# Kernel tuning notes

Hardware: AMD Instinct MI355X
Metric: run time of the kernel (lower is better)

The kernel has to match this reference:

```python
import jax, jax.numpy as jnp
import numpy as np

M_DIM = 1024
H_DIM = 1024
NEG = -1e9


def setup_inputs() -> dict:
    key = jax.random.key(0)
    ks = jax.random.split(key, 9)
    B, S = 4, 2048
    q = jax.random.normal(ks[0], (B, S, M_DIM), dtype=jnp.float32)
    k = jax.random.normal(ks[1], (B, S, M_DIM), dtype=jnp.float32)
    v = jax.random.normal(ks[2], (B, S, M_DIM), dtype=jnp.float32)
    attention_mask = jnp.ones((B, S), dtype=jnp.int32)
    sc = 1.0 / np.sqrt(M_DIM)
    Wq_w = jax.random.normal(ks[3], (H_DIM, M_DIM), dtype=jnp.float32) * sc
    Wq_b = jnp.zeros((H_DIM,), dtype=jnp.float32)
    Wk_w = jax.random.normal(ks[4], (H_DIM, M_DIM), dtype=jnp.float32) * sc
    Wk_b = jnp.zeros((H_DIM,), dtype=jnp.float32)
    Wv_w = jax.random.normal(ks[5], (H_DIM, M_DIM), dtype=jnp.float32) * sc
    Wv_b = jnp.zeros((H_DIM,), dtype=jnp.float32)
    return {"q": q, "k": k, "v": v, "attention_mask": attention_mask,
            "Wq_w": Wq_w, "Wq_b": Wq_b, "Wk_w": Wk_w, "Wk_b": Wk_b,
            "Wv_w": Wv_w, "Wv_b": Wv_b}


def reference(q, k, v, attention_mask, Wq_w, Wq_b, Wk_w, Wk_b, Wv_w, Wv_b):
    # Linear projections (torch Linear: x @ W.T + b)
    qh = jnp.einsum('bsm,hm->bsh', q, Wq_w) + Wq_b
    kh = jnp.einsum('bsm,hm->bsh', k, Wk_w) + Wk_b
    vh = jnp.einsum('bsm,hm->bsh', v, Wv_w) + Wv_b
    # Scaled dot-product scores: [B, Sq, Sk]
    scores = jnp.einsum('bqh,bkh->bqk', qh, kh) / jnp.sqrt(jnp.float32(H_DIM))
    # Padding mask: attention_mask [B, Sk] -> [B, 1, Sk]
    pad = attention_mask.astype(bool)[:, None, :]
    scores = jnp.where(pad, scores, NEG)
    # Causal mask (apply_mask=True)
    Sq, Sk = scores.shape[1], scores.shape[2]
    causal = jnp.tril(jnp.ones((Sq, Sk), dtype=bool))
    scores = jnp.where(causal[None, :, :], scores, NEG)
    attn = jax.nn.softmax(scores, axis=-1)
    out = jnp.einsum('bqk,bkh->bqh', attn, vh)
    # dropout is identity in eval mode
    return out
```

## Files before the change

### kernel.cpp

```cpp
#include <hip/hip_runtime.h>
#include <stdint.h>


typedef __attribute__((ext_vector_type(8))) short s8v;
typedef __attribute__((ext_vector_type(4))) float f4v;

__device__ __forceinline__ unsigned short f2bf(float f) {
    union { float f; unsigned u; } v; v.f = f;
    unsigned u = v.u;
    u = u + 0x7fffu + ((u >> 16) & 1u);
    return (unsigned short)(u >> 16);
}

__device__ __forceinline__ void gld_lds16(const void* gptr, void* lptr) {
    __builtin_amdgcn_global_load_lds(
        (const __attribute__((address_space(1))) unsigned int*)(uintptr_t)gptr,
        (__attribute__((address_space(3))) unsigned int*)(unsigned int)(uintptr_t)lptr,
        16, 0, 0);
}

__global__ __launch_bounds__(256) void convert_all(
    const float* __restrict__ q, const float* __restrict__ k, const float* __restrict__ v,
    const float* __restrict__ wq, const float* __restrict__ wk, const float* __restrict__ wv,
    unsigned short* __restrict__ qb, unsigned short* __restrict__ kb, unsigned short* __restrict__ vb,
    unsigned short* __restrict__ wqb, unsigned short* __restrict__ wkb, unsigned short* __restrict__ wvb,
    float* __restrict__ l)
{
    int b = blockIdx.x;
    if (b >= 27648) {
        int li = (b - 27648) * 256 + threadIdx.x;
        l[li] = 0.f;
        return;
    }
    const float* src; unsigned short* dst; int blk;
    if (b < 8192)       { src = q;  dst = qb;  blk = b; }
    else if (b < 16384) { src = k;  dst = kb;  blk = b - 8192; }
    else if (b < 24576) { src = v;  dst = vb;  blk = b - 16384; }
    else if (b < 25600) { src = wq; dst = wqb; blk = b - 24576; }
    else if (b < 26624) { src = wk; dst = wkb; blk = b - 25600; }
    else                { src = wv; dst = wvb; blk = b - 26624; }
    size_t idx = (size_t)blk * 1024 + (size_t)threadIdx.x * 4;
    float4 f = *(const float4*)(src + idx);
    ushort4 o = make_ushort4(f2bf(f.x), f2bf(f.y), f2bf(f.z), f2bf(f.w));
    *(ushort4*)(dst + idx) = o;
}

__device__ __forceinline__ void gemm_tiles(
    const unsigned short* __restrict__ A, int lda,
    const unsigned short* __restrict__ Bt, int ldb,
    int m0, int n0, int kTiles,
    unsigned short* As, unsigned short* Bs,
    f4v acc[4][4])
{
    const int t    = threadIdx.x;
    const int lane = t & 63;
    const int wave = t >> 6;
    const int wm   = (wave >> 1) * 64;
    const int wn   = (wave & 1) * 64;
    const int l15  = lane & 15;
    const int quad = lane >> 4;

    const int c0 = t, c1 = t + 256;
    unsigned short* As0 = As + (c0 & ~63) * 8;
    unsigned short* As1 = As + (c1 & ~63) * 8;
    unsigned short* Bs0 = Bs + (c0 & ~63) * 8;
    unsigned short* Bs1 = Bs + (c1 & ~63) * 8;
    const unsigned short* Ag0 = A  + (size_t)(m0 + (c0 >> 2)) * lda + (c0 & 3) * 8;
    const unsigned short* Ag1 = A  + (size_t)(m0 + (c1 >> 2)) * lda + (c1 & 3) * 8;
    const unsigned short* Bg0 = Bt + (size_t)(n0 + (c0 >> 2)) * ldb + (c0 & 3) * 8;
    const unsigned short* Bg1 = Bt + (size_t)(n0 + (c1 >> 2)) * ldb + (c1 & 3) * 8;

    const unsigned short* a_base = As + quad * 8;
    const unsigned short* b_base = Bs + quad * 8;

    gld_lds16(Ag0, As0);
    gld_lds16(Ag1, As1);
    gld_lds16(Bg0, Bs0);
    gld_lds16(Bg1, Bs1);

    for (int kt = 0; kt < kTiles; ++kt) {
        __syncthreads();
        Ag0 += 32; Ag1 += 32; Bg0 += 32; Bg1 += 32;
        if (kt + 1 < kTiles) {
            const int nb = ((kt + 1) & 1) * 4096;
            gld_lds16(Ag0, As0 + nb);
            gld_lds16(Ag1, As1 + nb);
            gld_lds16(Bg0, Bs0 + nb);
            gld_lds16(Bg1, Bs1 + nb);
        }
        const int cb = (kt & 1) * 4096;
        s8v af[4], bf[4];
        #pragma unroll
        for (int i = 0; i < 4; ++i)
            af[i] = *(const s8v*)(a_base + cb + (wm + i * 16 + l15) * 32);
        #pragma unroll
        for (int j = 0; j < 4; ++j)
            bf[j] = *(const s8v*)(b_base + cb + (wn + j * 16 + l15) * 32);
        #pragma unroll
        for (int i = 0; i < 4; ++i)
            #pragma unroll
            for (int j = 0; j < 4; ++j)
                acc[i][j] = __builtin_amdgcn_mfma_f32_16x16x32_bf16(af[i], bf[j], acc[i][j], 0, 0, 0);
    }
}

#define ACC_INIT  f4v acc[4][4]; { f4v z = {0.f,0.f,0.f,0.f}; \
    _Pragma("unroll") for (int i = 0; i < 4; ++i) \
    _Pragma("unroll") for (int j = 0; j < 4; ++j) acc[i][j] = z; }

#define LANE_VARS \
    const int lane = threadIdx.x & 63; const int wave = threadIdx.x >> 6; \
    const int wm = (wave >> 1) * 64;  const int wn = (wave & 1) * 64; \
    const int l15 = lane & 15;        const int quad = lane >> 4;

__global__ __launch_bounds__(512, 2) void proj_kernel(
    const unsigned short* __restrict__ qb, const unsigned short* __restrict__ wqb,
    const float* __restrict__ bq, unsigned short* __restrict__ QH,
    const unsigned short* __restrict__ kb, const unsigned short* __restrict__ wkb,
    const float* __restrict__ bk, unsigned short* __restrict__ KH,
    const unsigned short* __restrict__ vb, const unsigned short* __restrict__ wvb,
    const float* __restrict__ bv, unsigned short* __restrict__ VHT)
{
    const int z = blockIdx.z;
    const unsigned short* X; const unsigned short* W; const float* bias; unsigned short* Y;
    if (z == 0)      { X = qb; W = wqb; bias = bq; Y = QH; }
    else if (z == 1) { X = kb; W = wkb; bias = bk; Y = KH; }
    else             { X = vb; W = wvb; bias = bv; Y = VHT; }

    __shared__ __align__(16) unsigned short As[2 * 256 * 64];
    __shared__ __align__(16) unsigned short Bs[2 * 256 * 64];

    const int t    = threadIdx.x;
    const int lane = t & 63;
    const int w    = t >> 6;
    const int wm   = (w >> 2) * 128;
    const int wn   = (w & 3) * 64;
    const int l15  = lane & 15;
    const int quad = lane >> 4;
    const int m0   = blockIdx.x * 256;
    const int n0   = blockIdx.y * 256;
    enum { KT = 16 };

    const int r0 = t >> 3;
    const int sw = (t & 7) ^ (r0 & 7);
    const unsigned short* gA = X + (size_t)(m0 + r0) * 1024 + sw * 8;
    const unsigned short* gB = W + (size_t)(n0 + r0) * 1024 + sw * 8;
    unsigned short* lA = As + (t & ~63) * 8;
    unsigned short* lB = Bs + (t & ~63) * 8;

#define PSTAGE_A(b, h, kt) { \
    gld_lds16(gA + (size_t)(h) * 131072 + (kt) * 64,         lA + (b) * 16384 + (h) * 8192); \
    gld_lds16(gA + (size_t)(h) * 131072 + 65536 + (kt) * 64, lA + (b) * 16384 + (h) * 8192 + 4096); }
#define PSTAGE_B(b, h, kt) { \
    gld_lds16(gB + (size_t)(h) * 131072 + (kt) * 64,         lB + (b) * 16384 + (h) * 8192); \
    gld_lds16(gB + (size_t)(h) * 131072 + 65536 + (kt) * 64, lB + (b) * 16384 + (h) * 8192 + 4096); }

    const int aoff = (wm + l15) * 64;
    const int boff = (wn + l15) * 64;
    const int seg0 = ((quad    ) ^ (l15 & 7)) * 8;
    const int seg1 = ((quad | 4) ^ (l15 & 7)) * 8;

    f4v acc[8][4];
    { f4v zz = {0.f, 0.f, 0.f, 0.f};
      #pragma unroll
      for (int i = 0; i < 8; ++i)
        #pragma unroll
        for (int j = 0; j < 4; ++j) acc[i][j] = zz; }
    s8v a[8], b0[4], b1[4];

    PSTAGE_A(0, 0, 0); PSTAGE_A(0, 1, 0); PSTAGE_B(0, 0, 0); PSTAGE_B(0, 1, 0);
    PSTAGE_B(1, 0, 1); PSTAGE_A(1, 0, 1);
    asm volatile("s_waitcnt vmcnt(4)" ::: "memory");
    __builtin_amdgcn_s_barrier();

    for (int kt = 0; kt < KT; ++kt) {
        const int p  = kt & 1;
        const int np = p ^ 1;
        const unsigned short* Ar = As + p * 16384 + aoff;
        const unsigned short* Br = Bs + p * 16384 + boff;

        #pragma unroll
        for (int i = 0; i < 4; ++i) {
            a[i * 2]     = *(const s8v*)(Ar + i * 1024 + seg0);
            a[i * 2 + 1] = *(const s8v*)(Ar + i * 1024 + seg1);
        }
        #pragma unroll
        for (int j = 0; j < 2; ++j) {
            b0[j * 2]     = *(const s8v*)(Br + j * 1024 + seg0);
            b0[j * 2 + 1] = *(const s8v*)(Br + j * 1024 + seg1);
        }
        #pragma unroll
        for (int j = 0; j < 2; ++j) {
            b1[j * 2]     = *(const s8v*)(Br + 2048 + j * 1024 + seg0);
            b1[j * 2 + 1] = *(const s8v*)(Br + 2048 + j * 1024 + seg1);
        }
        if (kt + 1 < KT) PSTAGE_A(np, 1, kt + 1);
        __builtin_amdgcn_s_setprio(1);
        #pragma unroll
        for (int i = 0; i < 4; ++i)
            #pragma unroll
            for (int j = 0; j < 2; ++j) {
                acc[i][j] = __builtin_amdgcn_mfma_f32_16x16x32_bf16(a[i*2],   b0[j*2],   acc[i][j], 0, 0, 0);
                acc[i][j] = __builtin_amdgcn_mfma_f32_16x16x32_bf16(a[i*2+1], b0[j*2+1], acc[i][j], 0, 0, 0);
            }
        __builtin_amdgcn_s_setprio(0);
        if (kt + 1 < KT) PSTAGE_B(np, 1, kt + 1);
        __builtin_amdgcn_s_setprio(1);
        #pragma unroll
        for (int i = 0; i < 4; ++i)
            #pragma unroll
            for (int j = 0; j < 2; ++j) {
                acc[i][2+j] = __builtin_amdgcn_mfma_f32_16x16x32_bf16(a[i*2],   b1[j*2],   acc[i][2+j], 0, 0, 0);
                acc[i][2+j] = __builtin_amdgcn_mfma_f32_16x16x32_bf16(a[i*2+1], b1[j*2+1], acc[i][2+j], 0, 0, 0);
            }
        __builtin_amdgcn_s_setprio(0);
        #pragma unroll
        for (int i = 0; i < 4; ++i) {
            a[i * 2]     = *(const s8v*)(Ar + 4096 + i * 1024 + seg0);
            a[i * 2 + 1] = *(const s8v*)(Ar + 4096 + i * 1024 + seg1);
        }
        __builtin_amdgcn_s_barrier();
        if (kt + 2 < KT) PSTAGE_B(p, 0, kt + 2);
        __builtin_amdgcn_s_setprio(1);
        #pragma unroll
        for (int i = 0; i < 4; ++i)
            #pragma unroll
            for (int j = 0; j < 2; ++j) {
                acc[4+i][2+j] = __builtin_amdgcn_mfma_f32_16x16x32_bf16(a[i*2],   b1[j*2],   acc[4+i][2+j], 0, 0, 0);
                acc[4+i][2+j] = __builtin_amdgcn_mfma_f32_16x16x32_bf16(a[i*2+1], b1[j*2+1], acc[4+i][2+j], 0, 0, 0);
            }
        __builtin_amdgcn_s_setprio(0);
        __builtin_amdgcn_s_barrier();
        if (kt + 2 < KT) PSTAGE_A(p, 0, kt + 2);
        __builtin_amdgcn_s_setprio(1);
        #pragma unroll
        for (int i = 0; i < 4; ++i)
            #pragma unroll
            for (int j = 0; j < 2; ++j) {
                acc[4+i][j] = __builtin_amdgcn_mfma_f32_16x16x32_bf16(a[i*2],   b0[j*2],   acc[4+i][j], 0, 0, 0);
                acc[4+i][j] = __builtin_amdgcn_mfma_f32_16x16x32_bf16(a[i*2+1], b0[j*2+1], acc[4+i][j], 0, 0, 0);
            }
        __builtin_amdgcn_s_setprio(0);
        if (kt + 2 < KT) { asm volatile("s_waitcnt vmcnt(4)" ::: "memory"); }
        else             { asm volatile("s_waitcnt vmcnt(0)" ::: "memory"); }
        __builtin_amdgcn_s_barrier();
    }
#undef PSTAGE_A
#undef PSTAGE_B

    #pragma unroll
    for (int ig = 0; ig < 8; ++ig) {
        int row = m0 + wm + ig * 16 + quad * 4;
        #pragma unroll
        for (int jg = 0; jg < 4; ++jg) {
            int col = n0 + wn + jg * 16 + l15;
            float bvv = bias[col];
            if (z != 2) {
                #pragma unroll
                for (int r = 0; r < 4; ++r)
                    Y[(size_t)(row + r) * 1024 + col] = f2bf(acc[ig][jg][r] + bvv);
            } else {
                int bb = row >> 11;
                int s  = row & 2047;
                ushort4 o = make_ushort4(f2bf(acc[ig][jg][0] + bvv), f2bf(acc[ig][jg][1] + bvv),
                                         f2bf(acc[ig][jg][2] + bvv), f2bf(acc[ig][jg][3] + bvv));
                *(ushort4*)(Y + (size_t)bb * (1024 * 2048) + (size_t)col * 2048 + s) = o;
            }
        }
    }
}

__global__ __launch_bounds__(256) void score_kernel(
    const unsigned short* __restrict__ QH, const unsigned short* __restrict__ KH,
    const int* __restrict__ mask, unsigned short* __restrict__ P, float* __restrict__ lsum)
{
    const int b = blockIdx.y;
    int tq = blockIdx.x;
    int qt = 0;
    while ((qt + 1) * (qt + 2) / 2 <= tq) ++qt;
    const int kt = tq - qt * (qt + 1) / 2;

    __shared__ __align__(16) unsigned short As[2 * 128 * 32];
    __shared__ __align__(16) unsigned short Bs[2 * 128 * 32];
    const unsigned short* A  = QH + (size_t)b * 2048 * 1024;
    const unsigned short* Bt = KH + (size_t)b * 2048 * 1024;
    unsigned short* Pb = P + (size_t)b * 2048 * 2048;
    float* lb = lsum + b * 2048;
    const int* mb = mask + b * 2048;
    const int m0 = qt * 128, n0 = kt * 128;
    ACC_INIT;
    gemm_tiles(A, 1024, Bt, 1024, m0, n0, 32, As, Bs, acc);
    LANE_VARS;
    float rs[4][4];
    #pragma unroll
    for (int i = 0; i < 4; ++i)
        #pragma unroll
        for (int r = 0; r < 4; ++r) rs[i][r] = 0.f;
    #pragma unroll
    for (int i = 0; i < 4; ++i) {
        int qbase = m0 + wm + i * 16 + quad * 4;
        #pragma unroll
        for (int j = 0; j < 4; ++j) {
            int kg = n0 + wn + j * 16 + l15;
            int mv = mb[kg];
            #pragma unroll
            for (int r = 0; r < 4; ++r) {
                float s = acc[i][j][r] * 0.03125f;
                float p = (mv && (kg <= qbase + r)) ? __expf(s) : 0.f;
                Pb[(size_t)(qbase + r) * 2048 + kg] = f2bf(p);
                rs[i][r] += p;
            }
        }
    }
    #pragma unroll
    for (int i = 0; i < 4; ++i)
        #pragma unroll
        for (int r = 0; r < 4; ++r) {
            float v_ = rs[i][r];
            v_ += __shfl_xor(v_, 1);
            v_ += __shfl_xor(v_, 2);
            v_ += __shfl_xor(v_, 4);
            v_ += __shfl_xor(v_, 8);
            if (l15 == 0)
                atomicAdd(&lb[m0 + wm + i * 16 + quad * 4 + r], v_);
        }
}

__constant__ int pv_qt[24] = {15,15, 7,14,14,13,13, 6,12,12,11,11, 5,10,10, 9, 9, 4, 8, 8, 3, 2, 1, 0};
__constant__ int pv_ks[24] = { 0,32, 0, 0,30, 0,28, 0, 0,26, 0,24, 0, 0,22, 0,20, 0, 0,18, 0, 0, 0, 0};
__constant__ int pv_kc[24] = {32,32,32,30,30,28,28,28,26,26,24,24,24,22,22,20,20,20,18,18,16,12, 8, 4};

__global__ __launch_bounds__(256) void pv_kernel(
    const unsigned short* __restrict__ P, const unsigned short* __restrict__ VHT,
    const float* __restrict__ lsum, float* __restrict__ Out, float* __restrict__ Part)
{
    const int nt = blockIdx.x, y = blockIdx.y, b = blockIdx.z;
    const int qt = pv_qt[y], kstart = pv_ks[y], kcount = pv_kc[y];

    __shared__ __align__(16) unsigned short As[2 * 128 * 32];
    __shared__ __align__(16) unsigned short Bs[2 * 128 * 32];
    const unsigned short* A  = P   + (size_t)b * 2048 * 2048 + (size_t)kstart * 32;
    const unsigned short* Bt = VHT + (size_t)b * 1024 * 2048 + (size_t)kstart * 32;
    const float* lb = lsum + b * 2048;
    const int m0 = qt * 128, n0 = nt * 128;
    ACC_INIT;
    gemm_tiles(A, 2048, Bt, 2048, m0, n0, kcount, As, Bs, acc);
    LANE_VARS;
    float* dst; int rowoff;
    if (kstart == 0) { dst = Out  + (size_t)b * 2048 * 1024; rowoff = 0; }
    else             { dst = Part + (size_t)b * 1024 * 1024; rowoff = -1024; }
    #pragma unroll
    for (int i = 0; i < 4; ++i) {
        int q0 = m0 + wm + i * 16 + quad * 4;
        float inv[4];
        #pragma unroll
        for (int r = 0; r < 4; ++r) inv[r] = 1.0f / lb[q0 + r];
        #pragma unroll
        for (int j = 0; j < 4; ++j) {
            int h = n0 + wn + j * 16 + l15;
            #pragma unroll
            for (int r = 0; r < 4; ++r)
                dst[(size_t)(q0 + r + rowoff) * 1024 + h] = acc[i][j][r] * inv[r];
        }
    }
}

__global__ __launch_bounds__(256) void add_partial(
    float4* __restrict__ Out4, const float4* __restrict__ Part4)
{
    int i = blockIdx.x * 256 + threadIdx.x;
    int b = i >> 18;
    int rem = i & 262143;
    int oi = b * 524288 + 262144 + rem;
    float4 o = Out4[oi], p = Part4[i];
    o.x += p.x; o.y += p.y; o.z += p.z; o.w += p.w;
    Out4[oi] = o;
}

extern "C" void kernel_launch(void* const* d_in, const int* in_sizes, int n_in,
                              void* d_out, int out_size, void* d_ws, size_t ws_size,
                              hipStream_t stream)
{
    const float* q    = (const float*)d_in[0];
    const float* k    = (const float*)d_in[1];
    const float* v    = (const float*)d_in[2];
    const int*   mask = (const int*)d_in[3];
    const float* Wq   = (const float*)d_in[4];
    const float* bq   = (const float*)d_in[5];
    const float* Wk   = (const float*)d_in[6];
    const float* bk   = (const float*)d_in[7];
    const float* Wv   = (const float*)d_in[8];
    const float* bv   = (const float*)d_in[9];
    float* out = (float*)d_out;

    char* ws = (char*)d_ws;
    size_t off = 0;
    auto take = [&](size_t bytes) { char* p = ws + off; off += (bytes + 255) & ~(size_t)255; return p; };
    unsigned short* qb  = (unsigned short*)take(8192ull * 1024 * 2);
    unsigned short* kb  = (unsigned short*)take(8192ull * 1024 * 2);
    unsigned short* vb  = (unsigned short*)take(8192ull * 1024 * 2);
    unsigned short* wqb = (unsigned short*)take(1024ull * 1024 * 2);
    unsigned short* wkb = (unsigned short*)take(1024ull * 1024 * 2);
    unsigned short* wvb = (unsigned short*)take(1024ull * 1024 * 2);
    unsigned short* QH  = (unsigned short*)take(8192ull * 1024 * 2);
    unsigned short* KH  = (unsigned short*)take(8192ull * 1024 * 2);
    unsigned short* VHT = (unsigned short*)take(8192ull * 1024 * 2);
    unsigned short* P   = (unsigned short*)take(4ull * 2048 * 2048 * 2);
    float*          l   = (float*)take(4ull * 2048 * 4);
    float*          Part = (float*)qb;

    convert_all<<<27680, 256, 0, stream>>>(q, k, v, Wq, Wk, Wv,
                                           qb, kb, vb, wqb, wkb, wvb, l);
    proj_kernel<<<dim3(32, 4, 3), 512, 0, stream>>>(qb, wqb, bq, QH,
                                                    kb, wkb, bk, KH,
                                                    vb, wvb, bv, VHT);
    score_kernel<<<dim3(136, 4), 256, 0, stream>>>(QH, KH, mask, P, l);
    pv_kernel<<<dim3(8, 24, 4), 256, 0, stream>>>(P, VHT, l, out, Part);
    add_partial<<<4096, 256, 0, stream>>>((float4*)out, (const float4*)Part);
}
```

Baseline: 304.8 us.

## Fuse fp32-to-bf16 activation conversion into projection GEMM A-tile loads

Removes the standalone conversion pass over q/k/v. The projection kernel now loads fp32 activations into registers, converts them to bf16 and writes the swizzled tiles to LDS itself, and the waitcnt schedule is adjusted to match. This avoids writing and re-reading 48MB of bf16 intermediates, at the cost of register-staged loads instead of direct global-to-LDS copies. It also doubles A global traffic inside the GEMM, since the same tiles are reread as fp32 by four N-blocks, and adds VALU conversion work in the main loop.

```diff
diff --git a/kernel.cpp b/kernel.cpp
--- a/kernel.cpp
+++ b/kernel.cpp
@@ -19,26 +19,21 @@
         16, 0, 0);
 }
 
-__global__ __launch_bounds__(256) void convert_all(
-    const float* __restrict__ q, const float* __restrict__ k, const float* __restrict__ v,
+__global__ __launch_bounds__(256) void convert_w(
     const float* __restrict__ wq, const float* __restrict__ wk, const float* __restrict__ wv,
-    unsigned short* __restrict__ qb, unsigned short* __restrict__ kb, unsigned short* __restrict__ vb,
-    unsigned short* __restrict__ wqb, unsigned short* __restrict__ wkb, unsigned short* __restrict__ wvb,
-    float* __restrict__ l)
+    unsigned short* __restrict__ wqb, unsigned short* __restrict__ wkb,
+    unsigned short* __restrict__ wvb, float* __restrict__ l)
 {
     int b = blockIdx.x;
-    if (b >= 27648) {
-        int li = (b - 27648) * 256 + threadIdx.x;
+    if (b >= 3072) {
+        int li = (b - 3072) * 256 + threadIdx.x;
         l[li] = 0.f;
         return;
     }
     const float* src; unsigned short* dst; int blk;
-    if (b < 8192)       { src = q;  dst = qb;  blk = b; }
-    else if (b < 16384) { src = k;  dst = kb;  blk = b - 8192; }
-    else if (b < 24576) { src = v;  dst = vb;  blk = b - 16384; }
-    else if (b < 25600) { src = wq; dst = wqb; blk = b - 24576; }
-    else if (b < 26624) { src = wk; dst = wkb; blk = b - 25600; }
-    else                { src = wv; dst = wvb; blk = b - 26624; }
+    if (b < 1024)       { src = wq; dst = wqb; blk = b; }
+    else if (b < 2048)  { src = wk; dst = wkb; blk = b - 1024; }
+    else                { src = wv; dst = wvb; blk = b - 2048; }
     size_t idx = (size_t)blk * 1024 + (size_t)threadIdx.x * 4;
     float4 f = *(const float4*)(src + idx);
     ushort4 o = make_ushort4(f2bf(f.x), f2bf(f.y), f2bf(f.z), f2bf(f.w));
@@ -114,18 +109,18 @@
     const int l15 = lane & 15;        const int quad = lane >> 4;
 
 __global__ __launch_bounds__(512, 2) void proj_kernel(
-    const unsigned short* __restrict__ qb, const unsigned short* __restrict__ wqb,
+    const float* __restrict__ qf, const unsigned short* __restrict__ wqb,
     const float* __restrict__ bq, unsigned short* __restrict__ QH,
-    const unsigned short* __restrict__ kb, const unsigned short* __restrict__ wkb,
+    const float* __restrict__ kf, const unsigned short* __restrict__ wkb,
     const float* __restrict__ bk, unsigned short* __restrict__ KH,
-    const unsigned short* __restrict__ vb, const unsigned short* __restrict__ wvb,
+    const float* __restrict__ vf, const unsigned short* __restrict__ wvb,
     const float* __restrict__ bv, unsigned short* __restrict__ VHT)
 {
     const int z = blockIdx.z;
-    const unsigned short* X; const unsigned short* W; const float* bias; unsigned short* Y;
-    if (z == 0)      { X = qb; W = wqb; bias = bq; Y = QH; }
-    else if (z == 1) { X = kb; W = wkb; bias = bk; Y = KH; }
-    else             { X = vb; W = wvb; bias = bv; Y = VHT; }
+    const float* X; const unsigned short* W; const float* bias; unsigned short* Y;
+    if (z == 0)      { X = qf; W = wqb; bias = bq; Y = QH; }
+    else if (z == 1) { X = kf; W = wkb; bias = bk; Y = KH; }
+    else             { X = vf; W = wvb; bias = bv; Y = VHT; }
 
     __shared__ __align__(16) unsigned short As[2 * 256 * 64];
     __shared__ __align__(16) unsigned short Bs[2 * 256 * 64];
@@ -143,14 +138,29 @@
 
     const int r0 = t >> 3;
     const int sw = (t & 7) ^ (r0 & 7);
-    const unsigned short* gA = X + (size_t)(m0 + r0) * 1024 + sw * 8;
-    const unsigned short* gB = W + (size_t)(n0 + r0) * 1024 + sw * 8;
-    unsigned short* lA = As + (t & ~63) * 8;
-    unsigned short* lB = Bs + (t & ~63) * 8;
-
-#define PSTAGE_A(b, h, kt) { \
-    gld_lds16(gA + (size_t)(h) * 131072 + (kt) * 64,         lA + (b) * 16384 + (h) * 8192); \
-    gld_lds16(gA + (size_t)(h) * 131072 + 65536 + (kt) * 64, lA + (b) * 16384 + (h) * 8192 + 4096); }
+    const float*          gAf = X + (size_t)(m0 + r0) * 1024 + sw * 8;
+    const unsigned short* gB  = W + (size_t)(n0 + r0) * 1024 + sw * 8;
+    unsigned short* lAw = As + (size_t)t * 8;
+    unsigned short* lB  = Bs + (t & ~63) * 8;
+
+    float4 rA0, rA1, rA2, rA3;
+
+#define PLOAD_A(h, kt) { \
+    const float* _p = gAf + (size_t)(h) * 131072 + (kt) * 64; \
+    rA0 = *(const float4*)(_p);         rA1 = *(const float4*)(_p + 4); \
+    rA2 = *(const float4*)(_p + 65536); rA3 = *(const float4*)(_p + 65536 + 4); }
+#define PWRITE_A(b, h) { \
+    unsigned short* _d = lAw + (b) * 16384 + (h) * 8192; \
+    s8v _v0, _v1; \
+    _v0[0] = (short)f2bf(rA0.x); _v0[1] = (short)f2bf(rA0.y); \
+    _v0[2] = (short)f2bf(rA0.z); _v0[3] = (short)f2bf(rA0.w); \
+    _v0[4] = (short)f2bf(rA1.x); _v0[5] = (short)f2bf(rA1.y); \
+    _v0[6] = (short)f2bf(rA1.z); _v0[7] = (short)f2bf(rA1.w); \
+    _v1[0] = (short)f2bf(rA2.x); _v1[1] = (short)f2bf(rA2.y); \
+    _v1[2] = (short)f2bf(rA2.z); _v1[3] = (short)f2bf(rA2.w); \
+    _v1[4] = (short)f2bf(rA3.x); _v1[5] = (short)f2bf(rA3.y); \
+    _v1[6] = (short)f2bf(rA3.z); _v1[7] = (short)f2bf(rA3.w); \
+    *(s8v*)(_d) = _v0;  *(s8v*)(_d + 4096) = _v1; }
 #define PSTAGE_B(b, h, kt) { \
     gld_lds16(gB + (size_t)(h) * 131072 + (kt) * 64,         lB + (b) * 16384 + (h) * 8192); \
     gld_lds16(gB + (size_t)(h) * 131072 + 65536 + (kt) * 64, lB + (b) * 16384 + (h) * 8192 + 4096); }
@@ -168,9 +178,16 @@
         for (int j = 0; j < 4; ++j) acc[i][j] = zz; }
     s8v a[8], b0[4], b1[4];
 
-    PSTAGE_A(0, 0, 0); PSTAGE_A(0, 1, 0); PSTAGE_B(0, 0, 0); PSTAGE_B(0, 1, 0);
-    PSTAGE_B(1, 0, 1); PSTAGE_A(1, 0, 1);
-    asm volatile("s_waitcnt vmcnt(4)" ::: "memory");
+    PLOAD_A(0, 0);
+    PSTAGE_B(0, 0, 0); PSTAGE_B(0, 1, 0);
+    PWRITE_A(0, 0);
+    PLOAD_A(1, 0);
+    PWRITE_A(0, 1);
+    PLOAD_A(0, 1);
+    PWRITE_A(1, 0);
+    PLOAD_A(1, 1);
+    PSTAGE_B(1, 0, 1);
+    asm volatile("s_waitcnt vmcnt(0) lgkmcnt(0)" ::: "memory");
     __builtin_amdgcn_s_barrier();
 
     for (int kt = 0; kt < KT; ++kt) {
@@ -194,7 +211,8 @@
             b1[j * 2]     = *(const s8v*)(Br + 2048 + j * 1024 + seg0);
             b1[j * 2 + 1] = *(const s8v*)(Br + 2048 + j * 1024 + seg1);
         }
-        if (kt + 1 < KT) PSTAGE_A(np, 1, kt + 1);
+        if (kt + 1 < KT) PWRITE_A(np, 1);
+        if (kt + 2 < KT) PLOAD_A(0, kt + 2);
         __builtin_amdgcn_s_setprio(1);
         #pragma unroll
         for (int i = 0; i < 4; ++i)
@@ -231,7 +249,7 @@
             }
         __builtin_amdgcn_s_setprio(0);
         __builtin_amdgcn_s_barrier();
-        if (kt + 2 < KT) PSTAGE_A(p, 0, kt + 2);
+        if (kt + 2 < KT) { PWRITE_A(p, 0); PLOAD_A(1, kt + 2); }
         __builtin_amdgcn_s_setprio(1);
         #pragma unroll
         for (int i = 0; i < 4; ++i)
@@ -241,11 +259,13 @@
                 acc[4+i][j] = __builtin_amdgcn_mfma_f32_16x16x32_bf16(a[i*2+1], b0[j*2+1], acc[4+i][j], 0, 0, 0);
             }
         __builtin_amdgcn_s_setprio(0);
-        if (kt + 2 < KT) { asm volatile("s_waitcnt vmcnt(4)" ::: "memory"); }
+        asm volatile("s_waitcnt lgkmcnt(0)" ::: "memory");
+        if (kt + 2 < KT) { asm volatile("s_waitcnt vmcnt(6)" ::: "memory"); }
         else             { asm volatile("s_waitcnt vmcnt(0)" ::: "memory"); }
         __builtin_amdgcn_s_barrier();
     }
-#undef PSTAGE_A
+#undef PLOAD_A
+#undef PWRITE_A
 #undef PSTAGE_B
 
     #pragma unroll
@@ -396,9 +416,6 @@
     char* ws = (char*)d_ws;
     size_t off = 0;
     auto take = [&](size_t bytes) { char* p = ws + off; off += (bytes + 255) & ~(size_t)255; return p; };
-    unsigned short* qb  = (unsigned short*)take(8192ull * 1024 * 2);
-    unsigned short* kb  = (unsigned short*)take(8192ull * 1024 * 2);
-    unsigned short* vb  = (unsigned short*)take(8192ull * 1024 * 2);
     unsigned short* wqb = (unsigned short*)take(1024ull * 1024 * 2);
     unsigned short* wkb = (unsigned short*)take(1024ull * 1024 * 2);
     unsigned short* wvb = (unsigned short*)take(1024ull * 1024 * 2);
@@ -407,13 +424,12 @@
     unsigned short* VHT = (unsigned short*)take(8192ull * 1024 * 2);
     unsigned short* P   = (unsigned short*)take(4ull * 2048 * 2048 * 2);
     float*          l   = (float*)take(4ull * 2048 * 4);
-    float*          Part = (float*)qb;
-
-    convert_all<<<27680, 256, 0, stream>>>(q, k, v, Wq, Wk, Wv,
-                                           qb, kb, vb, wqb, wkb, wvb, l);
-    proj_kernel<<<dim3(32, 4, 3), 512, 0, stream>>>(qb, wqb, bq, QH,
-                                                    kb, wkb, bk, KH,
-                                                    vb, wvb, bv, VHT);
+    float*          Part = (float*)take(4ull * 1024 * 1024 * 4);
+
+    convert_w<<<3104, 256, 0, stream>>>(Wq, Wk, Wv, wqb, wkb, wvb, l);
+    proj_kernel<<<dim3(32, 4, 3), 512, 0, stream>>>(q, wqb, bq, QH,
+                                                    k, wkb, bk, KH,
+                                                    v, wvb, bv, VHT);
     score_kernel<<<dim3(136, 4), 256, 0, stream>>>(QH, KH, mask, P, l);
     pv_kernel<<<dim3(8, 24, 4), 256, 0, stream>>>(P, VHT, l, out, Part);
     add_partial<<<4096, 256, 0, stream>>>((float4*)out, (const float4*)Part);
```

New measurement: 326.4 us. 7.1% more time.
